# Kernel optimization log

Measured on AMD Instinct MI355X. Metric: run time of the kernel, lower is better.

## Reference

```python
import jax, jax.numpy as jnp
import numpy as np

ATOM_FDIM = 35
BOND_FDIM = 5
MAX_NB = 15
HIDDEN = 512
DEPTH = 6
N_MOLS = 1024
ATOMS_PER_MOL = 32
N_ATOMS = N_MOLS * ATOMS_PER_MOL      # 32768
N_BONDS = 2 * N_ATOMS                  # 65536 (each bond appears in both directions)
N_MESS = 8192                          # tree messages (row 0 is the zero pad slot)
TOTAL_MSG = N_MESS + N_BONDS           # index space for agraph/bgraph


def setup_inputs() -> dict:
    key = jax.random.key(0)
    ks = jax.random.split(key, 8)
    fatoms = jax.random.normal(ks[0], (N_ATOMS, ATOM_FDIM), jnp.float32)
    fbonds = jax.random.normal(ks[1], (N_BONDS, ATOM_FDIM + BOND_FDIM), jnp.float32)
    agraph = jax.random.randint(ks[2], (N_ATOMS, MAX_NB), 0, TOTAL_MSG, dtype=jnp.int32)
    bgraph = jax.random.randint(ks[3], (N_BONDS, MAX_NB), 0, TOTAL_MSG, dtype=jnp.int32)
    # row 0 of the concatenated message table is the padding slot -> zero it
    tree_message = jax.random.normal(ks[4], (N_MESS, HIDDEN), jnp.float32).at[0].set(0.0)
    starts = jnp.arange(N_MOLS, dtype=jnp.int32) * ATOMS_PER_MOL
    scope = jnp.stack([starts, jnp.full((N_MOLS,), ATOMS_PER_MOL, jnp.int32)], axis=1)
    s_i = 1.0 / np.sqrt(ATOM_FDIM + BOND_FDIM)
    s_h = 1.0 / np.sqrt(HIDDEN)
    s_o = 1.0 / np.sqrt(ATOM_FDIM + HIDDEN)
    W_i = jax.random.normal(ks[5], (ATOM_FDIM + BOND_FDIM, HIDDEN), jnp.float32) * s_i
    W_h = jax.random.normal(ks[6], (HIDDEN, HIDDEN), jnp.float32) * s_h
    W_o = jax.random.normal(ks[7], (ATOM_FDIM + HIDDEN, HIDDEN), jnp.float32) * s_o
    b_o = jnp.zeros((HIDDEN,), jnp.float32)
    return {"fatoms": fatoms, "fbonds": fbonds, "agraph": agraph, "bgraph": bgraph,
            "scope": scope, "tree_message": tree_message,
            "W_i": W_i, "W_h": W_h, "W_o": W_o, "b_o": b_o}


def reference(fatoms, fbonds, agraph, bgraph, scope, tree_message, W_i, W_h, W_o, b_o):
    binput = fbonds @ W_i                         # [B, H]
    graph_message = jax.nn.relu(binput)

    def step(gm, _):
        message = jnp.concatenate([tree_message, gm], axis=0)   # [M+B, H]
        nei = message[bgraph].sum(axis=1)                       # gather-sum [B, H]
        return jax.nn.relu(binput + nei @ W_h), None

    graph_message, _ = jax.lax.scan(step, graph_message, None, length=DEPTH - 1)

    message = jnp.concatenate([tree_message, graph_message], axis=0)
    nei = message[agraph].sum(axis=1)             # [A, H]
    ainput = jnp.concatenate([fatoms, nei], axis=1)
    atom_hiddens = jax.nn.relu(ainput @ W_o + b_o)

    # scope is uniform (st = i*ATOMS_PER_MOL, le = ATOMS_PER_MOL) -> static segment ids
    seg = jnp.repeat(jnp.arange(N_MOLS), ATOMS_PER_MOL)
    sums = jax.ops.segment_sum(atom_hiddens, seg, num_segments=N_MOLS)
    return sums / scope[:, 1:].astype(atom_hiddens.dtype)
```

## Files before the change

### kernel.cpp

```cpp
#include <hip/hip_runtime.h>
#include <stdint.h>


#define MAX_NB 15
#define HID 512
#define NA 32768
#define NB 65536
#define NMESS 8192

typedef unsigned short u16;
typedef unsigned int u32;
typedef __bf16 bf16x8 __attribute__((ext_vector_type(8)));
typedef float f32x4 __attribute__((ext_vector_type(4)));

__device__ __forceinline__ u16 f2bf(float f) {
  u32 u = __builtin_bit_cast(u32, f);
  u32 r = (u + 0x7fffu + ((u >> 16) & 1u)) >> 16;
  return (u16)r;
}
__device__ __forceinline__ float bflo(u32 u) {
  return __builtin_bit_cast(float, u << 16);
}
__device__ __forceinline__ float bfhi(u32 u) {
  return __builtin_bit_cast(float, u & 0xffff0000u);
}

__device__ __forceinline__ void async16(const u16* g, u16* l) {
  __builtin_amdgcn_global_load_lds(
      (const __attribute__((address_space(1))) u32*)g,
      (__attribute__((address_space(3))) u32*)l, 16, 0, 0);
}

__global__ __launch_bounds__(256) void prep_kernel(
    const float* __restrict__ fbonds, const float* __restrict__ tree,
    const float* __restrict__ Wi, const float* __restrict__ Wh,
    const float* __restrict__ Wo, u16* __restrict__ msg,
    u16* __restrict__ fbpad, u16* __restrict__ wcat, u16* __restrict__ wo_t) {
  int t = blockIdx.x * 256 + threadIdx.x;
  const int N0 = NMESS * HID;
  const int N1 = NB * 64;
  const int N2 = 512 * 576;
  const int N3 = 512 * 576;
  if (t < N0) { msg[t] = f2bf(tree[t]); return; }
  t -= N0;
  if (t < N1) {
    int row = t >> 6, c = t & 63;
    fbpad[t] = (c < 40) ? f2bf(fbonds[row * 40 + c]) : (u16)0;
    return;
  }
  t -= N1;
  if (t < N2) {
    int n = t / 576, k = t - n * 576;
    float v = 0.f;
    if (k < 40) v = Wi[k * 512 + n];
    else if (k >= 64) v = Wh[(k - 64) * 512 + n];
    wcat[t] = f2bf(v);
    return;
  }
  t -= N2;
  if (t < N3) {
    int n = t / 576, k = t - n * 576;
    float v = 0.f;
    if (k < 512) v = Wo[(35 + k) * 512 + n];
    else if (k < 547) v = Wo[(k - 512) * 512 + n];
    wo_t[t] = f2bf(v);
    return;
  }
}

__global__ __launch_bounds__(256) void gather_bonds(
    const u16* __restrict__ msg, const int* __restrict__ bgraph,
    u16* __restrict__ nei) {
  const int xcd = blockIdx.x & 7;
  const int chunk = blockIdx.x >> 3;
  int row = xcd * (NB / 8) + chunk * 4 + (threadIdx.x >> 6);
  int lane = threadIdx.x & 63;
  const int* idxp = bgraph + row * MAX_NB;
  float acc[8] = {0, 0, 0, 0, 0, 0, 0, 0};
#pragma unroll
  for (int j = 0; j < MAX_NB; j++) {
    int id = idxp[j];
    uint4 v = *(const uint4*)(msg + (size_t)id * HID + lane * 8);
    acc[0] += bflo(v.x); acc[1] += bfhi(v.x);
    acc[2] += bflo(v.y); acc[3] += bfhi(v.y);
    acc[4] += bflo(v.z); acc[5] += bfhi(v.z);
    acc[6] += bflo(v.w); acc[7] += bfhi(v.w);
  }
  uint4 o;
  o.x = (u32)f2bf(acc[0]) | ((u32)f2bf(acc[1]) << 16);
  o.y = (u32)f2bf(acc[2]) | ((u32)f2bf(acc[3]) << 16);
  o.z = (u32)f2bf(acc[4]) | ((u32)f2bf(acc[5]) << 16);
  o.w = (u32)f2bf(acc[6]) | ((u32)f2bf(acc[7]) << 16);
  *(uint4*)(nei + (size_t)row * HID + lane * 8) = o;
}

__global__ __launch_bounds__(256) void gather_atoms(
    const u16* __restrict__ msg, const int* __restrict__ agraph,
    const float* __restrict__ fatoms, u16* __restrict__ ainput) {
  const int xcd = blockIdx.x & 7;
  const int chunk = blockIdx.x >> 3;
  int row = xcd * (NA / 8) + chunk * 4 + (threadIdx.x >> 6);
  int lane = threadIdx.x & 63;
  const int* idxp = agraph + row * MAX_NB;
  float acc[8] = {0, 0, 0, 0, 0, 0, 0, 0};
#pragma unroll
  for (int j = 0; j < MAX_NB; j++) {
    int id = idxp[j];
    uint4 v = *(const uint4*)(msg + (size_t)id * HID + lane * 8);
    acc[0] += bflo(v.x); acc[1] += bfhi(v.x);
    acc[2] += bflo(v.y); acc[3] += bfhi(v.y);
    acc[4] += bflo(v.z); acc[5] += bfhi(v.z);
    acc[6] += bflo(v.w); acc[7] += bfhi(v.w);
  }
  uint4 o;
  o.x = (u32)f2bf(acc[0]) | ((u32)f2bf(acc[1]) << 16);
  o.y = (u32)f2bf(acc[2]) | ((u32)f2bf(acc[3]) << 16);
  o.z = (u32)f2bf(acc[4]) | ((u32)f2bf(acc[5]) << 16);
  o.w = (u32)f2bf(acc[6]) | ((u32)f2bf(acc[7]) << 16);
  u16* arow = ainput + (size_t)row * 576;
  *(uint4*)(arow + lane * 8) = o;
  float tv = (lane < 35) ? fatoms[(size_t)row * 35 + lane] : 0.f;
  arow[512 + lane] = f2bf(tv);
}

template <int EPI>
__global__ __launch_bounds__(256) void gemm_k(
    const u16* __restrict__ A1, int s1, int kSplit,
    const u16* __restrict__ A2, const u16* __restrict__ Bt, int Bstride, int K,
    int mtx, u16* __restrict__ msgout, const float* __restrict__ bo,
    const int* __restrict__ scope, float* __restrict__ out) {
  __shared__ __align__(16) u16 As[128 * 32];
  __shared__ __align__(16) u16 Bs[128 * 32];
  const int L = blockIdx.x;
  const int xcd = L & 7;
  const int q = L >> 3;
  const int mBase = (xcd * mtx + (q >> 2)) * 128;
  const int nBase = (q & 3) * 128;
  const int t = threadIdx.x;
  const int lane = t & 63;
  const int w = t >> 6;
  const int wm = w & 1, wn = w >> 1;
  const int r = t >> 2;
  const int c8 = (t & 3) * 8;
  const int q8 = (lane >> 4) * 8;
  const int l15 = lane & 15;

  f32x4 acc[4][4];
#pragma unroll
  for (int i = 0; i < 4; i++)
#pragma unroll
    for (int j = 0; j < 4; j++)
#pragma unroll
      for (int rg = 0; rg < 4; rg++) acc[i][j][rg] = 0.f;

  for (int kb = 0; kb < K; kb += 32) {
    const u16* Ab;
    int Astr, kOff;
    if (kb < kSplit) { Ab = A1; Astr = s1; kOff = kb; }
    else { Ab = A2; Astr = 512; kOff = kb - kSplit; }
    __syncthreads();
    async16(Ab + (size_t)(mBase + r) * Astr + kOff + c8, As + r * 32 + c8);
    async16(Ab + (size_t)(mBase + r + 64) * Astr + kOff + c8,
            As + (r + 64) * 32 + c8);
    async16(Bt + (size_t)(nBase + r) * Bstride + kb + c8, Bs + r * 32 + c8);
    async16(Bt + (size_t)(nBase + r + 64) * Bstride + kb + c8,
            Bs + (r + 64) * 32 + c8);
    __syncthreads();
    bf16x8 av[4], bv[4];
#pragma unroll
    for (int i = 0; i < 4; i++)
      av[i] = *(const bf16x8*)(As + (wm * 64 + i * 16 + l15) * 32 + q8);
#pragma unroll
    for (int j = 0; j < 4; j++)
      bv[j] = *(const bf16x8*)(Bs + (wn * 64 + j * 16 + l15) * 32 + q8);
#pragma unroll
    for (int i = 0; i < 4; i++)
#pragma unroll
      for (int j = 0; j < 4; j++)
        acc[i][j] = __builtin_amdgcn_mfma_f32_16x16x32_bf16(av[i], bv[j],
                                                            acc[i][j], 0, 0, 0);
  }

  if (EPI == 2) {
#pragma unroll
    for (int m = 0; m < 2; m++) {
      int mol = (mBase + wm * 64 + m * 32) >> 5;
      float inv_le = 1.0f / (float)scope[mol * 2 + 1];
#pragma unroll
      for (int j = 0; j < 4; j++) {
        int col = nBase + wn * 64 + j * 16 + l15;
        float bias = bo[col];
        float s = 0.f;
#pragma unroll
        for (int i = 2 * m; i < 2 * m + 2; i++)
#pragma unroll
          for (int rg = 0; rg < 4; rg++)
            s += fmaxf(acc[i][j][rg] + bias, 0.f);
        s += __shfl_xor(s, 16, 64);
        s += __shfl_xor(s, 32, 64);
        if (lane < 16) out[(size_t)mol * HID + col] = s * inv_le;
      }
    }
  } else {
#pragma unroll
    for (int i = 0; i < 4; i++) {
      int row = mBase + wm * 64 + i * 16 + (lane >> 4) * 4;
#pragma unroll
      for (int j = 0; j < 4; j++) {
        int col = nBase + wn * 64 + j * 16 + l15;
#pragma unroll
        for (int rg = 0; rg < 4; rg++) {
          size_t gi = (size_t)(row + rg) * HID + col;
          msgout[(size_t)NMESS * HID + gi] = f2bf(fmaxf(acc[i][j][rg], 0.f));
        }
      }
    }
  }
}

extern "C" void kernel_launch(void* const* d_in, const int* in_sizes, int n_in,
                              void* d_out, int out_size, void* d_ws,
                              size_t ws_size, hipStream_t stream) {
  const float* fatoms = (const float*)d_in[0];
  const float* fbonds = (const float*)d_in[1];
  const int* agraph = (const int*)d_in[2];
  const int* bgraph = (const int*)d_in[3];
  const int* scope = (const int*)d_in[4];
  const float* tree = (const float*)d_in[5];
  const float* Wi = (const float*)d_in[6];
  const float* Wh = (const float*)d_in[7];
  const float* Wo = (const float*)d_in[8];
  const float* bo = (const float*)d_in[9];
  float* out = (float*)d_out;

  char* ws = (char*)d_ws;
  u16* msg = (u16*)(ws);
  u16* nei = (u16*)(ws + 75497472ull);
  u16* fbpad = (u16*)(ws + 142606336ull);
  u16* wcat = (u16*)(ws + 150994944ull);
  u16* wo_t = (u16*)(ws + 151584768ull);
  u16* ainput = nei;

  prep_kernel<<<35072, 256, 0, stream>>>(fbonds, tree, Wi, Wh, Wo, msg, fbpad,
                                         wcat, wo_t);

  gemm_k<0><<<2048, 256, 0, stream>>>(fbpad, 64, 64, nullptr, wcat, 576, 64,
                                      64, msg, nullptr, nullptr, nullptr);
  for (int d = 0; d < 5; d++) {
    gather_bonds<<<NB / 4, 256, 0, stream>>>(msg, bgraph, nei);
    gemm_k<0><<<2048, 256, 0, stream>>>(fbpad, 64, 64, nei, wcat, 576, 576,
                                        64, msg, nullptr, nullptr, nullptr);
  }
  gather_atoms<<<NA / 4, 256, 0, stream>>>(msg, agraph, fatoms, ainput);
  gemm_k<2><<<1024, 256, 0, stream>>>(ainput, 576, 576, nullptr, wo_t, 576,
                                      576, 32, nullptr, bo, scope, out);
}
```

Baseline: 1.243 ms.

## Double-buffer GEMM shared tiles and batch neighbor loads in gather kernels

The GEMM kernel now keeps two LDS buffers for the A and B tiles. It issues the async copy of the next K-slice before running the MFMAs on the current one, so the pipeline has one barrier per iteration instead of two. Global-to-LDS latency is meant to overlap with matrix math, at the cost of twice the shared memory per block, which may reduce occupancy. Both gather kernels first load all 15 indices and all 15 neighbor rows into registers, then sum them. This raises the number of memory requests in flight and costs more registers.

```diff
diff --git a/kernel.cpp b/kernel.cpp
--- a/kernel.cpp
+++ b/kernel.cpp
@@ -76,15 +76,20 @@
   int row = xcd * (NB / 8) + chunk * 4 + (threadIdx.x >> 6);
   int lane = threadIdx.x & 63;
   const int* idxp = bgraph + row * MAX_NB;
+  int ids[MAX_NB];
+#pragma unroll
+  for (int j = 0; j < MAX_NB; j++) ids[j] = idxp[j];
+  uint4 v[MAX_NB];
+#pragma unroll
+  for (int j = 0; j < MAX_NB; j++)
+    v[j] = *(const uint4*)(msg + (size_t)ids[j] * HID + lane * 8);
   float acc[8] = {0, 0, 0, 0, 0, 0, 0, 0};
 #pragma unroll
   for (int j = 0; j < MAX_NB; j++) {
-    int id = idxp[j];
-    uint4 v = *(const uint4*)(msg + (size_t)id * HID + lane * 8);
-    acc[0] += bflo(v.x); acc[1] += bfhi(v.x);
-    acc[2] += bflo(v.y); acc[3] += bfhi(v.y);
-    acc[4] += bflo(v.z); acc[5] += bfhi(v.z);
-    acc[6] += bflo(v.w); acc[7] += bfhi(v.w);
+    acc[0] += bflo(v[j].x); acc[1] += bfhi(v[j].x);
+    acc[2] += bflo(v[j].y); acc[3] += bfhi(v[j].y);
+    acc[4] += bflo(v[j].z); acc[5] += bfhi(v[j].z);
+    acc[6] += bflo(v[j].w); acc[7] += bfhi(v[j].w);
   }
   uint4 o;
   o.x = (u32)f2bf(acc[0]) | ((u32)f2bf(acc[1]) << 16);
@@ -102,15 +107,20 @@
   int row = xcd * (NA / 8) + chunk * 4 + (threadIdx.x >> 6);
   int lane = threadIdx.x & 63;
   const int* idxp = agraph + row * MAX_NB;
+  int ids[MAX_NB];
+#pragma unroll
+  for (int j = 0; j < MAX_NB; j++) ids[j] = idxp[j];
+  uint4 v[MAX_NB];
+#pragma unroll
+  for (int j = 0; j < MAX_NB; j++)
+    v[j] = *(const uint4*)(msg + (size_t)ids[j] * HID + lane * 8);
   float acc[8] = {0, 0, 0, 0, 0, 0, 0, 0};
 #pragma unroll
   for (int j = 0; j < MAX_NB; j++) {
-    int id = idxp[j];
-    uint4 v = *(const uint4*)(msg + (size_t)id * HID + lane * 8);
-    acc[0] += bflo(v.x); acc[1] += bfhi(v.x);
-    acc[2] += bflo(v.y); acc[3] += bfhi(v.y);
-    acc[4] += bflo(v.z); acc[5] += bfhi(v.z);
-    acc[6] += bflo(v.w); acc[7] += bfhi(v.w);
+    acc[0] += bflo(v[j].x); acc[1] += bfhi(v[j].x);
+    acc[2] += bflo(v[j].y); acc[3] += bfhi(v[j].y);
+    acc[4] += bflo(v[j].z); acc[5] += bfhi(v[j].z);
+    acc[6] += bflo(v[j].w); acc[7] += bfhi(v[j].w);
   }
   uint4 o;
   o.x = (u32)f2bf(acc[0]) | ((u32)f2bf(acc[1]) << 16);
@@ -129,8 +139,8 @@
     const u16* __restrict__ A2, const u16* __restrict__ Bt, int Bstride, int K,
     int mtx, u16* __restrict__ msgout, const float* __restrict__ bo,
     const int* __restrict__ scope, float* __restrict__ out) {
-  __shared__ __align__(16) u16 As[128 * 32];
-  __shared__ __align__(16) u16 Bs[128 * 32];
+  __shared__ __align__(16) u16 As[2][128 * 32];
+  __shared__ __align__(16) u16 Bs[2][128 * 32];
   const int L = blockIdx.x;
   const int xcd = L & 7;
   const int q = L >> 3;
@@ -153,32 +163,39 @@
 #pragma unroll
       for (int rg = 0; rg < 4; rg++) acc[i][j][rg] = 0.f;
 
-  for (int kb = 0; kb < K; kb += 32) {
+  auto stage = [&](int c, int kb) {
     const u16* Ab;
     int Astr, kOff;
     if (kb < kSplit) { Ab = A1; Astr = s1; kOff = kb; }
     else { Ab = A2; Astr = 512; kOff = kb - kSplit; }
-    __syncthreads();
-    async16(Ab + (size_t)(mBase + r) * Astr + kOff + c8, As + r * 32 + c8);
+    async16(Ab + (size_t)(mBase + r) * Astr + kOff + c8, As[c] + r * 32 + c8);
     async16(Ab + (size_t)(mBase + r + 64) * Astr + kOff + c8,
-            As + (r + 64) * 32 + c8);
-    async16(Bt + (size_t)(nBase + r) * Bstride + kb + c8, Bs + r * 32 + c8);
+            As[c] + (r + 64) * 32 + c8);
+    async16(Bt + (size_t)(nBase + r) * Bstride + kb + c8, Bs[c] + r * 32 + c8);
     async16(Bt + (size_t)(nBase + r + 64) * Bstride + kb + c8,
-            Bs + (r + 64) * 32 + c8);
-    __syncthreads();
+            Bs[c] + (r + 64) * 32 + c8);
+  };
+
+  stage(0, 0);
+  __syncthreads();
+  int cur = 0;
+  for (int kb = 0; kb < K; kb += 32) {
+    if (kb + 32 < K) stage(cur ^ 1, kb + 32);
     bf16x8 av[4], bv[4];
 #pragma unroll
     for (int i = 0; i < 4; i++)
-      av[i] = *(const bf16x8*)(As + (wm * 64 + i * 16 + l15) * 32 + q8);
+      av[i] = *(const bf16x8*)(As[cur] + (wm * 64 + i * 16 + l15) * 32 + q8);
 #pragma unroll
     for (int j = 0; j < 4; j++)
-      bv[j] = *(const bf16x8*)(Bs + (wn * 64 + j * 16 + l15) * 32 + q8);
+      bv[j] = *(const bf16x8*)(Bs[cur] + (wn * 64 + j * 16 + l15) * 32 + q8);
 #pragma unroll
     for (int i = 0; i < 4; i++)
 #pragma unroll
       for (int j = 0; j < 4; j++)
         acc[i][j] = __builtin_amdgcn_mfma_f32_16x16x32_bf16(av[i], bv[j],
                                                             acc[i][j], 0, 0, 0);
+    __syncthreads();
+    cur ^= 1;
   }
 
   if (EPI == 2) {
```

Result: no change. 1.221 ms (-1.7%).

## Overlap neighbor gathers with message GEMMs via ping-pong buffers and mixed kernels

Applied to the files above, without the earlier changes.

Graph messages now ping-pong between two buffers, so the gather for one depth can run while that depth's GEMM writes the other buffer. A new mixed kernel runs GEMM tiles on rows already gathered while other blocks gather the remaining row chunks, followed by a GEMM on the leftover tiles. The GEMM kernels gain double-buffered LDS with a prefetch of the next K slice. The bond-feature pad buffer is replaced by a compact stride-40 copy. The overlap path only runs when the workspace is large enough, which adds complexity and depends on hand-picked chunk split points.

```diff
diff --git a/kernel.cpp b/kernel.cpp
--- a/kernel.cpp
+++ b/kernel.cpp
@@ -7,6 +7,7 @@
 #define NA 32768
 #define NB 65536
 #define NMESS 8192
+#define GAPE 33554432u
 
 typedef unsigned short u16;
 typedef unsigned int u32;
@@ -34,22 +35,16 @@
 __global__ __launch_bounds__(256) void prep_kernel(
     const float* __restrict__ fbonds, const float* __restrict__ tree,
     const float* __restrict__ Wi, const float* __restrict__ Wh,
-    const float* __restrict__ Wo, u16* __restrict__ msg,
-    u16* __restrict__ fbpad, u16* __restrict__ wcat, u16* __restrict__ wo_t) {
+    const float* __restrict__ Wo, u16* __restrict__ tab,
+    u16* __restrict__ fbc, u16* __restrict__ wcat, u16* __restrict__ wo_t) {
   int t = blockIdx.x * 256 + threadIdx.x;
   const int N0 = NMESS * HID;
-  const int N1 = NB * 64;
-  const int N2 = 512 * 576;
-  const int N3 = 512 * 576;
-  if (t < N0) { msg[t] = f2bf(tree[t]); return; }
+  if (t < N0) { tab[t] = f2bf(tree[t]); return; }
   t -= N0;
-  if (t < N1) {
-    int row = t >> 6, c = t & 63;
-    fbpad[t] = (c < 40) ? f2bf(fbonds[row * 40 + c]) : (u16)0;
-    return;
-  }
-  t -= N1;
-  if (t < N2) {
+  const int N1 = NB * 40;
+  if (t < N1 + 32) { fbc[t] = (t < N1) ? f2bf(fbonds[t]) : (u16)0; return; }
+  t -= N1 + 32;
+  if (t < 576 * 512) {
     int n = t / 576, k = t - n * 576;
     float v = 0.f;
     if (k < 40) v = Wi[k * 512 + n];
@@ -57,8 +52,8 @@
     wcat[t] = f2bf(v);
     return;
   }
-  t -= N2;
-  if (t < N3) {
+  t -= 576 * 512;
+  if (t < 576 * 512) {
     int n = t / 576, k = t - n * 576;
     float v = 0.f;
     if (k < 512) v = Wo[(35 + k) * 512 + n];
@@ -69,8 +64,8 @@
 }
 
 __global__ __launch_bounds__(256) void gather_bonds(
-    const u16* __restrict__ msg, const int* __restrict__ bgraph,
-    u16* __restrict__ nei) {
+    const u16* __restrict__ tab, const int* __restrict__ bgraph,
+    u16* __restrict__ nei, u32 pOff) {
   const int xcd = blockIdx.x & 7;
   const int chunk = blockIdx.x >> 3;
   int row = xcd * (NB / 8) + chunk * 4 + (threadIdx.x >> 6);
@@ -80,7 +75,8 @@
 #pragma unroll
   for (int j = 0; j < MAX_NB; j++) {
     int id = idxp[j];
-    uint4 v = *(const uint4*)(msg + (size_t)id * HID + lane * 8);
+    u32 off = (u32)id * HID + (id >= NMESS ? pOff : 0u);
+    uint4 v = *(const uint4*)(tab + (size_t)off + lane * 8);
     acc[0] += bflo(v.x); acc[1] += bfhi(v.x);
     acc[2] += bflo(v.y); acc[3] += bfhi(v.y);
     acc[4] += bflo(v.z); acc[5] += bfhi(v.z);
@@ -95,8 +91,8 @@
 }
 
 __global__ __launch_bounds__(256) void gather_atoms(
-    const u16* __restrict__ msg, const int* __restrict__ agraph,
-    const float* __restrict__ fatoms, u16* __restrict__ ainput) {
+    const u16* __restrict__ tab, const int* __restrict__ agraph,
+    const float* __restrict__ fatoms, u16* __restrict__ ainput, u32 pOff) {
   const int xcd = blockIdx.x & 7;
   const int chunk = blockIdx.x >> 3;
   int row = xcd * (NA / 8) + chunk * 4 + (threadIdx.x >> 6);
@@ -106,7 +102,8 @@
 #pragma unroll
   for (int j = 0; j < MAX_NB; j++) {
     int id = idxp[j];
-    uint4 v = *(const uint4*)(msg + (size_t)id * HID + lane * 8);
+    u32 off = (u32)id * HID + (id >= NMESS ? pOff : 0u);
+    uint4 v = *(const uint4*)(tab + (size_t)off + lane * 8);
     acc[0] += bflo(v.x); acc[1] += bfhi(v.x);
     acc[2] += bflo(v.y); acc[3] += bfhi(v.y);
     acc[4] += bflo(v.z); acc[5] += bfhi(v.z);
@@ -126,15 +123,15 @@
 template <int EPI>
 __global__ __launch_bounds__(256) void gemm_k(
     const u16* __restrict__ A1, int s1, int kSplit,
-    const u16* __restrict__ A2, const u16* __restrict__ Bt, int Bstride, int K,
-    int mtx, u16* __restrict__ msgout, const float* __restrict__ bo,
+    const u16* __restrict__ A2, const u16* __restrict__ Bt, int K, int mtx,
+    int tileStart, u16* __restrict__ gw, const float* __restrict__ bo,
     const int* __restrict__ scope, float* __restrict__ out) {
-  __shared__ __align__(16) u16 As[128 * 32];
-  __shared__ __align__(16) u16 Bs[128 * 32];
+  __shared__ __align__(16) u16 As[2][128 * 32];
+  __shared__ __align__(16) u16 Bs[2][128 * 32];
   const int L = blockIdx.x;
   const int xcd = L & 7;
   const int q = L >> 3;
-  const int mBase = (xcd * mtx + (q >> 2)) * 128;
+  const int mBase = (xcd * mtx + tileStart + (q >> 2)) * 128;
   const int nBase = (q & 3) * 128;
   const int t = threadIdx.x;
   const int lane = t & 63;
@@ -153,32 +150,39 @@
 #pragma unroll
       for (int rg = 0; rg < 4; rg++) acc[i][j][rg] = 0.f;
 
-  for (int kb = 0; kb < K; kb += 32) {
+  auto stage = [&](int c, int kb) {
     const u16* Ab;
     int Astr, kOff;
     if (kb < kSplit) { Ab = A1; Astr = s1; kOff = kb; }
     else { Ab = A2; Astr = 512; kOff = kb - kSplit; }
-    __syncthreads();
-    async16(Ab + (size_t)(mBase + r) * Astr + kOff + c8, As + r * 32 + c8);
+    async16(Ab + (size_t)(mBase + r) * Astr + kOff + c8, As[c] + r * 32 + c8);
     async16(Ab + (size_t)(mBase + r + 64) * Astr + kOff + c8,
-            As + (r + 64) * 32 + c8);
-    async16(Bt + (size_t)(nBase + r) * Bstride + kb + c8, Bs + r * 32 + c8);
-    async16(Bt + (size_t)(nBase + r + 64) * Bstride + kb + c8,
-            Bs + (r + 64) * 32 + c8);
-    __syncthreads();
+            As[c] + (r + 64) * 32 + c8);
+    async16(Bt + (size_t)(nBase + r) * 576 + kb + c8, Bs[c] + r * 32 + c8);
+    async16(Bt + (size_t)(nBase + r + 64) * 576 + kb + c8,
+            Bs[c] + (r + 64) * 32 + c8);
+  };
+
+  stage(0, 0);
+  __syncthreads();
+  int cur = 0;
+  for (int kb = 0; kb < K; kb += 32) {
+    if (kb + 32 < K) stage(cur ^ 1, kb + 32);
     bf16x8 av[4], bv[4];
 #pragma unroll
     for (int i = 0; i < 4; i++)
-      av[i] = *(const bf16x8*)(As + (wm * 64 + i * 16 + l15) * 32 + q8);
+      av[i] = *(const bf16x8*)(As[cur] + (wm * 64 + i * 16 + l15) * 32 + q8);
 #pragma unroll
     for (int j = 0; j < 4; j++)
-      bv[j] = *(const bf16x8*)(Bs + (wn * 64 + j * 16 + l15) * 32 + q8);
+      bv[j] = *(const bf16x8*)(Bs[cur] + (wn * 64 + j * 16 + l15) * 32 + q8);
 #pragma unroll
     for (int i = 0; i < 4; i++)
 #pragma unroll
       for (int j = 0; j < 4; j++)
         acc[i][j] = __builtin_amdgcn_mfma_f32_16x16x32_bf16(av[i], bv[j],
                                                             acc[i][j], 0, 0, 0);
+    __syncthreads();
+    cur ^= 1;
   }
 
   if (EPI == 2) {
@@ -211,9 +215,148 @@
 #pragma unroll
         for (int rg = 0; rg < 4; rg++) {
           size_t gi = (size_t)(row + rg) * HID + col;
-          msgout[(size_t)NMESS * HID + gi] = f2bf(fmaxf(acc[i][j][rg], 0.f));
+          gw[gi] = f2bf(fmaxf(acc[i][j][rg], 0.f));
         }
       }
+    }
+  }
+}
+
+template <int PHASE>
+__global__ __launch_bounds__(512, 4) void mixed(
+    const u16* __restrict__ tab, u32 pOff, u16* __restrict__ gw,
+    u16* __restrict__ nei, const u16* __restrict__ fbc,
+    const u16* __restrict__ W, const int* __restrict__ graph,
+    const float* __restrict__ fatoms, const float* __restrict__ bo,
+    const int* __restrict__ scope, float* __restrict__ out, int nGemmBlk,
+    int chunkStart) {
+  __shared__ __align__(16) u16 As[2][128 * 32];
+  __shared__ __align__(16) u16 Bs[2][128 * 32];
+  constexpr int MTX = PHASE ? 32 : 64;
+  constexpr int ROWQ = PHASE ? (NA / 8) : (NB / 8);
+  const int xcd = blockIdx.x & 7;
+  const int u = blockIdx.x >> 3;
+  const int t = threadIdx.x;
+  const int lane = t & 63;
+
+  if (u < nGemmBlk) {
+    const int tile = u >> 2, nb = u & 3;
+    const int mBase = (xcd * MTX + tile) * 128;
+    const int nBase = nb * 128;
+    const int w = t >> 6;
+    const int wm = w & 1, wn = w >> 1;
+    const int r = t >> 2;
+    const int c8 = (t & 3) * 8;
+    const int q8 = (lane >> 4) * 8;
+    const int l15 = lane & 15;
+    const int K = 576;
+
+    f32x4 acc[4][2];
+#pragma unroll
+    for (int i = 0; i < 4; i++)
+#pragma unroll
+      for (int j = 0; j < 2; j++)
+#pragma unroll
+        for (int rg = 0; rg < 4; rg++) acc[i][j][rg] = 0.f;
+
+    auto stage = [&](int c, int kb) {
+      const u16* Ab;
+      int Astr, kOff;
+      if (PHASE == 0) {
+        if (kb < 64) { Ab = fbc; Astr = 40; kOff = kb; }
+        else { Ab = nei; Astr = 512; kOff = kb - 64; }
+      } else {
+        Ab = nei; Astr = 576; kOff = kb;
+      }
+      async16(Ab + (size_t)(mBase + r) * Astr + kOff + c8, As[c] + r * 32 + c8);
+      async16(W + (size_t)(nBase + r) * 576 + kb + c8, Bs[c] + r * 32 + c8);
+    };
+
+    stage(0, 0);
+    __syncthreads();
+    int cur = 0;
+    for (int kb = 0; kb < K; kb += 32) {
+      if (kb + 32 < K) stage(cur ^ 1, kb + 32);
+      bf16x8 av[4], bv[2];
+#pragma unroll
+      for (int i = 0; i < 4; i++)
+        av[i] = *(const bf16x8*)(As[cur] + (wm * 64 + i * 16 + l15) * 32 + q8);
+#pragma unroll
+      for (int j = 0; j < 2; j++)
+        bv[j] = *(const bf16x8*)(Bs[cur] + (wn * 32 + j * 16 + l15) * 32 + q8);
+#pragma unroll
+      for (int i = 0; i < 4; i++)
+#pragma unroll
+        for (int j = 0; j < 2; j++)
+          acc[i][j] = __builtin_amdgcn_mfma_f32_16x16x32_bf16(av[i], bv[j],
+                                                              acc[i][j], 0, 0, 0);
+      __syncthreads();
+      cur ^= 1;
+    }
+
+    if (PHASE == 1) {
+#pragma unroll
+      for (int m = 0; m < 2; m++) {
+        int mol = (mBase + wm * 64 + m * 32) >> 5;
+        float inv_le = 1.0f / (float)scope[mol * 2 + 1];
+#pragma unroll
+        for (int j = 0; j < 2; j++) {
+          int col = nBase + wn * 32 + j * 16 + l15;
+          float bias = bo[col];
+          float s = 0.f;
+#pragma unroll
+          for (int i = 2 * m; i < 2 * m + 2; i++)
+#pragma unroll
+            for (int rg = 0; rg < 4; rg++)
+              s += fmaxf(acc[i][j][rg] + bias, 0.f);
+          s += __shfl_xor(s, 16, 64);
+          s += __shfl_xor(s, 32, 64);
+          if (lane < 16) out[(size_t)mol * HID + col] = s * inv_le;
+        }
+      }
+    } else {
+#pragma unroll
+      for (int i = 0; i < 4; i++) {
+        int row = mBase + wm * 64 + i * 16 + (lane >> 4) * 4;
+#pragma unroll
+        for (int j = 0; j < 2; j++) {
+          int col = nBase + wn * 32 + j * 16 + l15;
+#pragma unroll
+          for (int rg = 0; rg < 4; rg++) {
+            size_t gi = (size_t)(row + rg) * HID + col;
+            gw[gi] = f2bf(fmaxf(acc[i][j][rg], 0.f));
+          }
+        }
+      }
+    }
+  } else {
+    const int g = u - nGemmBlk;
+    const int w = t >> 6;
+    const int row = xcd * ROWQ + chunkStart * 128 + g * 8 + w;
+    const int* idxp = graph + row * MAX_NB;
+    float acc[8] = {0, 0, 0, 0, 0, 0, 0, 0};
+#pragma unroll
+    for (int j = 0; j < MAX_NB; j++) {
+      int id = idxp[j];
+      u32 off = (u32)id * HID + (id >= NMESS ? pOff : 0u);
+      uint4 v = *(const uint4*)(tab + (size_t)off + lane * 8);
+      acc[0] += bflo(v.x); acc[1] += bfhi(v.x);
+      acc[2] += bflo(v.y); acc[3] += bfhi(v.y);
+      acc[4] += bflo(v.z); acc[5] += bfhi(v.z);
+      acc[6] += bflo(v.w); acc[7] += bfhi(v.w);
+    }
+    uint4 o;
+    o.x = (u32)f2bf(acc[0]) | ((u32)f2bf(acc[1]) << 16);
+    o.y = (u32)f2bf(acc[2]) | ((u32)f2bf(acc[3]) << 16);
+    o.z = (u32)f2bf(acc[4]) | ((u32)f2bf(acc[5]) << 16);
+    o.w = (u32)f2bf(acc[6]) | ((u32)f2bf(acc[7]) << 16);
+    if (PHASE == 1) {
+      u16* arow = nei + (size_t)row * 576;
+      *(uint4*)(arow + lane * 8) = o;
+      float tv = (lane < 35) ? fatoms[(size_t)row * 35 + lane] : 0.f;
+      arow[512 + lane] = f2bf(tv);
+    } else {
+      *(uint4*)(nei + (size_t)row * HID + lane * 8) = o;
     }
   }
 }
@@ -233,25 +376,50 @@
   const float* bo = (const float*)d_in[9];
   float* out = (float*)d_out;
 
-  char* ws = (char*)d_ws;
-  u16* msg = (u16*)(ws);
-  u16* nei = (u16*)(ws + 75497472ull);
-  u16* fbpad = (u16*)(ws + 142606336ull);
-  u16* wcat = (u16*)(ws + 150994944ull);
-  u16* wo_t = (u16*)(ws + 151584768ull);
-  u16* ainput = nei;
-
-  prep_kernel<<<35072, 256, 0, stream>>>(fbonds, tree, Wi, Wh, Wo, msg, fbpad,
-                                         wcat, wo_t);
-
-  gemm_k<0><<<2048, 256, 0, stream>>>(fbpad, 64, 64, nullptr, wcat, 576, 64,
-                                      64, msg, nullptr, nullptr, nullptr);
-  for (int d = 0; d < 5; d++) {
-    gather_bonds<<<NB / 4, 256, 0, stream>>>(msg, bgraph, nei);
-    gemm_k<0><<<2048, 256, 0, stream>>>(fbpad, 64, 64, nei, wcat, 576, 576,
-                                        64, msg, nullptr, nullptr, nullptr);
-  }
-  gather_atoms<<<NA / 4, 256, 0, stream>>>(msg, agraph, fatoms, ainput);
-  gemm_k<2><<<1024, 256, 0, stream>>>(ainput, 576, 576, nullptr, wo_t, 576,
-                                      576, 32, nullptr, bo, scope, out);
-}
+  const int ov = ws_size >= 216137792ull;
+  u16* tab = (u16*)d_ws;
+  u16* graphA = tab + (size_t)NMESS * HID;
+  u16* nei = graphA + (size_t)(ov ? 2 : 1) * GAPE;
+  u16* fbc = nei + (size_t)GAPE;
+  u16* wcat = fbc + ((size_t)NB * 40 + 32);
+  u16* wo_t = wcat + 576 * 512;
+
+  const int prepTot = NMESS * HID + NB * 40 + 32 + 2 * 576 * 512;
+  prep_kernel<<<(prepTot + 255) / 256, 256, 0, stream>>>(fbonds, tree, Wi, Wh,
+                                                         Wo, tab, fbc, wcat,
+                                                         wo_t);
+
+  gemm_k<0><<<2048, 256, 0, stream>>>(fbc, 40, 64, nullptr, wcat, 64, 64, 0,
+                                      graphA, nullptr, nullptr, nullptr);
+
+  if (ov) {
+    const int C1 = 45;
+    const int CA = 22;
+    for (int d = 0; d < 5; d++) {
+      u32 pOff = (u32)(d & 1) * GAPE;
+      u16* gw = graphA + (size_t)((d + 1) & 1) * GAPE;
+      gather_bonds<<<8 * C1 * 32, 256, 0, stream>>>(tab, bgraph, nei, pOff);
+      mixed<0><<<8 * (C1 * 4 + (64 - C1) * 16), 512, 0, stream>>>(
+          tab, pOff, gw, nei, fbc, wcat, bgraph, nullptr, nullptr, nullptr,
+          nullptr, C1 * 4, C1);
+      gemm_k<0><<<8 * (64 - C1) * 4, 256, 0, stream>>>(
+          fbc, 40, 64, nei, wcat, 576, 64, C1, gw, nullptr, nullptr, nullptr);
+    }
+    gather_atoms<<<8 * CA * 32, 256, 0, stream>>>(tab, agraph, fatoms, nei,
+                                                  GAPE);
+    mixed<1><<<8 * (CA * 4 + (32 - CA) * 16), 512, 0, stream>>>(
+        tab, GAPE, nullptr, nei, nullptr, wo_t, agraph, fatoms, bo, scope, out,
+        CA * 4, CA);
+    gemm_k<2><<<8 * (32 - CA) * 4, 256, 0, stream>>>(
+        nei, 576, 576, nullptr, wo_t, 576, 32, CA, nullptr, bo, scope, out);
+  } else {
+    for (int d = 0; d < 5; d++) {
+      gather_bonds<<<NB / 4, 256, 0, stream>>>(tab, bgraph, nei, 0u);
+      gemm_k<0><<<2048, 256, 0, stream>>>(fbc, 40, 64, nei, wcat, 576, 64, 0,
+                                          graphA, nullptr, nullptr, nullptr);
+    }
+    gather_atoms<<<NA / 4, 256, 0, stream>>>(tab, agraph, fatoms, nei, 0u);
+    gemm_k<2><<<1024, 256, 0, stream>>>(nei, 576, 576, nullptr, wo_t, 576, 32,
+                                        0, nullptr, bo, scope, out);
+  }
+}
```

Result: no change. 1.231 ms (-1.0%).
